# Kernel tuning notes

Hardware: AMD Instinct MI355X
Metric: run time of the kernel (lower is better)

The kernel has to match this reference:

```python
import jax, jax.numpy as jnp
import numpy as np

B, T, N = 16, 2048, 1024
SPIKE_RATE = 0.02


def setup_inputs() -> dict:
    key = jax.random.key(0)
    k1, k2 = jax.random.split(key)
    u = jax.random.uniform(k1, (B, T, N), dtype=jnp.float32)
    output_spikes = (u < SPIKE_RATE).astype(jnp.float32)
    target_cv = jax.random.uniform(k2, (N,), dtype=jnp.float32)
    return {"output_spikes": output_spikes, "target_cv": target_cv}


def reference(output_spikes, target_cv):
    # Flatten (batch[, patterns], time) into one long trial-concatenated train per neuron,
    # matching output_spikes[:, :, n].reshape(-1) in the torch loop.
    n_neurons = output_spikes.shape[-1]
    s = output_spikes.reshape(-1, n_neurons)          # (Ttot, N)
    Ttot = s.shape[0]
    m = s > 0                                          # spike mask
    times = jnp.arange(Ttot, dtype=jnp.float32)[:, None]

    # Previous spike time at each position via exclusive cumulative max of spike times.
    st = jnp.where(m, times, -1.0)                     # (Ttot, N)
    cmax = jax.lax.cummax(st, axis=0)
    prev = jnp.concatenate([jnp.full((1, n_neurons), -1.0, st.dtype), cmax[:-1]], axis=0)

    # ISI gap at every spike that has a predecessor: gap = t - prev_spike_time.
    gmask = m & (prev >= 0.0)
    gaps = jnp.where(gmask, times - prev, 0.0)

    k = jnp.sum(m, axis=0).astype(jnp.float32)         # spike count per neuron
    n_isi = k - 1.0                                    # number of ISIs
    sum_g = jnp.sum(gaps, axis=0)
    sum_g2 = jnp.sum(gaps * gaps, axis=0)

    mean_isi = sum_g / jnp.maximum(n_isi, 1.0)
    # torch.Tensor.std is unbiased (divide by n_isi - 1)
    var = (sum_g2 - n_isi * mean_isi * mean_isi) / jnp.maximum(n_isi - 1.0, 1.0)
    std = jnp.sqrt(jnp.maximum(var, 0.0))

    # NaN in torch corresponds here to: <3 spikes or mean_isi <= 0 -> excluded from loss.
    valid = (k >= 3.0) & (mean_isi > 0.0)
    cv = jnp.where(valid, std / jnp.where(mean_isi > 0.0, mean_isi, 1.0), 0.0)
    sq = jnp.where(valid, (cv - target_cv) ** 2, 0.0)
    nvalid = jnp.sum(valid.astype(jnp.float32))
    return jnp.where(nvalid > 0.0, jnp.sum(sq) / jnp.maximum(nvalid, 1.0), 0.0)
```

## Files before the change

kernel.cpp:

```cpp
#include <hip/hip_runtime.h>
#include <math.h>

#define TTOT   32768
#define NNEUR  1024
#define NCHUNK 512
#define SUBLEN 16
#define NC4    (NNEUR / 4)

struct SegState { float cnt, first, last, g2; };

__device__ __forceinline__ SegState seg_combine(const SegState& a, const SegState& b) {
    if (a.cnt == 0.0f) return b;
    if (b.cnt == 0.0f) return a;
    SegState r;
    float gap = b.first - a.last;
    r.cnt   = a.cnt + b.cnt;
    r.first = a.first;
    r.last  = b.last;
    r.g2    = a.g2 + b.g2 + gap * gap;
    return r;
}

__global__ __launch_bounds__(256) void k_scan(const float* __restrict__ s,
                                              float4* __restrict__ wstate) {
    const int tid  = threadIdx.x;
    const int ccol = tid & 63;
    const int ysl  = tid >> 6;
    const int col4 = blockIdx.x * 64 + ccol;
    const int t0   = blockIdx.y * 64 + ysl * SUBLEN;

    const float4* s4 = reinterpret_cast<const float4*>(s);

    float cnt[4]   = {0.f, 0.f, 0.f, 0.f};
    float first[4] = {-1.f, -1.f, -1.f, -1.f};
    float last[4]  = {-1.f, -1.f, -1.f, -1.f};
    float g2[4]    = {0.f, 0.f, 0.f, 0.f};

    #pragma unroll
    for (int i = 0; i < SUBLEN; ++i) {
        const int t = t0 + i;
        const float4 v = s4[(size_t)t * NC4 + col4];
        const float tt = (float)t;
        float vals[4] = {v.x, v.y, v.z, v.w};
        #pragma unroll
        for (int j = 0; j < 4; ++j) {
            if (vals[j] > 0.0f) {
                if (cnt[j] > 0.0f) {
                    float g = tt - last[j];
                    g2[j] += g * g;
                } else {
                    first[j] = tt;
                }
                last[j] = tt;
                cnt[j] += 1.0f;
            }
        }
    }

    __shared__ float4 lds[4][64][4];
    #pragma unroll
    for (int j = 0; j < 4; ++j)
        lds[ysl][ccol][j] = make_float4(cnt[j], first[j], last[j], g2[j]);
    __syncthreads();

    if (ysl == 0) {
        #pragma unroll
        for (int j = 0; j < 4; ++j) {
            float4 a = lds[0][ccol][j];
            SegState st = {a.x, a.y, a.z, a.w};
            #pragma unroll
            for (int y = 1; y < 4; ++y) {
                float4 b = lds[y][ccol][j];
                SegState sb = {b.x, b.y, b.z, b.w};
                st = seg_combine(st, sb);
            }
            wstate[(size_t)blockIdx.y * NNEUR + col4 * 4 + j] =
                make_float4(st.cnt, st.first, st.last, st.g2);
        }
    }
}

__global__ __launch_bounds__(256) void k_combine(const float4* __restrict__ wstate,
                                                 const float* __restrict__ target,
                                                 float* __restrict__ outsq,
                                                 float* __restrict__ outvalid) {
    const int tid  = threadIdx.x;
    const int lane = tid & 63;
    const int w    = tid >> 6;
    const int n    = blockIdx.x * 4 + w;

    SegState st = {0.f, -1.f, -1.f, 0.f};
    #pragma unroll
    for (int j = 0; j < NCHUNK / 64; ++j) {
        int c = lane * (NCHUNK / 64) + j;
        float4 a = wstate[(size_t)c * NNEUR + n];
        SegState sb = {a.x, a.y, a.z, a.w};
        st = seg_combine(st, sb);
    }
    for (int off = 1; off < 64; off <<= 1) {
        SegState o;
        o.cnt   = __shfl_down(st.cnt,   off);
        o.first = __shfl_down(st.first, off);
        o.last  = __shfl_down(st.last,  off);
        o.g2    = __shfl_down(st.g2,    off);
        if ((lane & (2 * off - 1)) == 0) st = seg_combine(st, o);
    }

    if (lane == 0) {
        float k     = st.cnt;
        float n_isi = k - 1.0f;
        float sum_g = (k > 0.0f) ? (st.last - st.first) : 0.0f;
        float mean  = sum_g / fmaxf(n_isi, 1.0f);
        float var   = (st.g2 - n_isi * mean * mean) / fmaxf(n_isi - 1.0f, 1.0f);
        float sd    = sqrtf(fmaxf(var, 0.0f));
        bool valid  = (k >= 3.0f) && (mean > 0.0f);
        float cv    = valid ? sd / mean : 0.0f;
        float d     = cv - target[n];
        outsq[n]    = valid ? d * d : 0.0f;
        outvalid[n] = valid ? 1.0f : 0.0f;
    }
}

__global__ __launch_bounds__(256) void k_reduce(const float* __restrict__ outsq,
                                                const float* __restrict__ outvalid,
                                                float* __restrict__ out) {
    const int tid = threadIdx.x;
    float s = 0.f, v = 0.f;
    for (int i = tid; i < NNEUR; i += 256) {
        s += outsq[i];
        v += outvalid[i];
    }
    for (int off = 32; off > 0; off >>= 1) {
        s += __shfl_down(s, off);
        v += __shfl_down(v, off);
    }
    __shared__ float ls[4], lv[4];
    const int w = tid >> 6;
    if ((tid & 63) == 0) { ls[w] = s; lv[w] = v; }
    __syncthreads();
    if (tid == 0) {
        float S = ls[0] + ls[1] + ls[2] + ls[3];
        float V = lv[0] + lv[1] + lv[2] + lv[3];
        out[0] = (V > 0.0f) ? S / fmaxf(V, 1.0f) : 0.0f;
    }
}

extern "C" void kernel_launch(void* const* d_in, const int* in_sizes, int n_in,
                              void* d_out, int out_size, void* d_ws, size_t ws_size,
                              hipStream_t stream) {
    const float* spikes = (const float*)d_in[0];
    const float* target = (const float*)d_in[1];
    float* out = (float*)d_out;

    char* wsb = (char*)d_ws;
    float4* wstate   = (float4*)wsb;
    float*  outsq    = (float*)(wsb + (size_t)NCHUNK * NNEUR * sizeof(float4));
    float*  outvalid = outsq + NNEUR;

    dim3 g1(NNEUR / 256, NCHUNK);
    k_scan<<<g1, 256, 0, stream>>>(spikes, wstate);
    k_combine<<<NNEUR / 4, 256, 0, stream>>>(wstate, target, outsq, outvalid);
    k_reduce<<<1, 256, 0, stream>>>(outsq, outvalid, out);
}
```

Before: 40.98 us.

## Use larger time chunks per block to shrink intermediate state and combine work

Each scan block now covers 512 time steps with 1024 threads (16 sub-slices of 32 steps) instead of 64 steps with 256 threads. This cuts the per-chunk state written to the workspace by 8x, so the combine kernel reads only one state per lane and drops its serial pre-combine loop. The in-block merge now uses structure-of-arrays shared memory and spreads the 16-way combine over 256 threads. In exchange the grid has only 256 blocks, which may not keep all compute units busy or hide memory latency.

```diff
diff --git a/kernel.cpp b/kernel.cpp
--- a/kernel.cpp
+++ b/kernel.cpp
@@ -1,11 +1,12 @@
 #include <hip/hip_runtime.h>
 #include <math.h>
 
-#define TTOT   32768
-#define NNEUR  1024
-#define NCHUNK 512
-#define SUBLEN 16
-#define NC4    (NNEUR / 4)
+#define TTOT     32768
+#define NNEUR    1024
+#define NCHUNK   64
+#define CHUNKLEN 512
+#define SUBLEN   32
+#define NC4      (NNEUR / 4)
 
 struct SegState { float cnt, first, last, g2; };
 
@@ -21,13 +22,13 @@
     return r;
 }
 
-__global__ __launch_bounds__(256) void k_scan(const float* __restrict__ s,
-                                              float4* __restrict__ wstate) {
+__global__ __launch_bounds__(1024) void k_scan(const float* __restrict__ s,
+                                               float4* __restrict__ wstate) {
     const int tid  = threadIdx.x;
     const int ccol = tid & 63;
     const int ysl  = tid >> 6;
     const int col4 = blockIdx.x * 64 + ccol;
-    const int t0   = blockIdx.y * 64 + ysl * SUBLEN;
+    const int t0   = blockIdx.y * CHUNKLEN + ysl * SUBLEN;
 
     const float4* s4 = reinterpret_cast<const float4*>(s);
 
@@ -36,7 +37,7 @@
     float last[4]  = {-1.f, -1.f, -1.f, -1.f};
     float g2[4]    = {0.f, 0.f, 0.f, 0.f};
 
-    #pragma unroll
+    #pragma unroll 4
     for (int i = 0; i < SUBLEN; ++i) {
         const int t = t0 + i;
         const float4 v = s4[(size_t)t * NC4 + col4];
@@ -57,26 +58,27 @@
         }
     }
 
-    __shared__ float4 lds[4][64][4];
+    __shared__ float lcnt[16][4][64], lfirst[16][4][64], llast[16][4][64], lg2[16][4][64];
     #pragma unroll
-    for (int j = 0; j < 4; ++j)
-        lds[ysl][ccol][j] = make_float4(cnt[j], first[j], last[j], g2[j]);
+    for (int j = 0; j < 4; ++j) {
+        lcnt  [ysl][j][ccol] = cnt[j];
+        lfirst[ysl][j][ccol] = first[j];
+        llast [ysl][j][ccol] = last[j];
+        lg2   [ysl][j][ccol] = g2[j];
+    }
     __syncthreads();
 
-    if (ysl == 0) {
+    if (tid < 256) {
+        const int c = tid >> 2;
+        const int j = tid & 3;
+        SegState st = {lcnt[0][j][c], lfirst[0][j][c], llast[0][j][c], lg2[0][j][c]};
         #pragma unroll
-        for (int j = 0; j < 4; ++j) {
-            float4 a = lds[0][ccol][j];
-            SegState st = {a.x, a.y, a.z, a.w};
-            #pragma unroll
-            for (int y = 1; y < 4; ++y) {
-                float4 b = lds[y][ccol][j];
-                SegState sb = {b.x, b.y, b.z, b.w};
-                st = seg_combine(st, sb);
-            }
-            wstate[(size_t)blockIdx.y * NNEUR + col4 * 4 + j] =
-                make_float4(st.cnt, st.first, st.last, st.g2);
+        for (int y = 1; y < 16; ++y) {
+            SegState b = {lcnt[y][j][c], lfirst[y][j][c], llast[y][j][c], lg2[y][j][c]};
+            st = seg_combine(st, b);
         }
+        wstate[(size_t)blockIdx.y * NNEUR + blockIdx.x * 256 + tid] =
+            make_float4(st.cnt, st.first, st.last, st.g2);
     }
 }
 
@@ -89,14 +91,9 @@
     const int w    = tid >> 6;
     const int n    = blockIdx.x * 4 + w;
 
-    SegState st = {0.f, -1.f, -1.f, 0.f};
-    #pragma unroll
-    for (int j = 0; j < NCHUNK / 64; ++j) {
-        int c = lane * (NCHUNK / 64) + j;
-        float4 a = wstate[(size_t)c * NNEUR + n];
-        SegState sb = {a.x, a.y, a.z, a.w};
-        st = seg_combine(st, sb);
-    }
+    float4 a = wstate[(size_t)lane * NNEUR + n];
+    SegState st = {a.x, a.y, a.z, a.w};
+
     for (int off = 1; off < 64; off <<= 1) {
         SegState o;
         o.cnt   = __shfl_down(st.cnt,   off);
@@ -158,7 +155,7 @@
     float*  outvalid = outsq + NNEUR;
 
     dim3 g1(NNEUR / 256, NCHUNK);
-    k_scan<<<g1, 256, 0, stream>>>(spikes, wstate);
+    k_scan<<<g1, 1024, 0, stream>>>(spikes, wstate);
     k_combine<<<NNEUR / 4, 256, 0, stream>>>(wstate, target, outsq, outvalid);
     k_reduce<<<1, 256, 0, stream>>>(outsq, outvalid, out);
 }
```

After: 35.65 us. 13.0% less time.
